# Kernel tuning notes

Measured on AMD Instinct MI355X. Metric: run time of the kernel, lower is better.

## Reference

```python
import jax, jax.numpy as jnp
import numpy as np

B, T, C = 16, 1024, 768
H = 12
D = C // H  # 64 head dim


def setup_inputs() -> dict:
    key = jax.random.key(0)
    k1, k2, k3, k4, k5 = jax.random.split(key, 5)
    s = 0.02
    return {
        "x": jax.random.normal(k1, (B, T, C), dtype=jnp.float32),
        "w_attn": jax.random.normal(k2, (C, 3 * C), dtype=jnp.float32) * s,
        "b_attn": jax.random.normal(k3, (3 * C,), dtype=jnp.float32) * s,
        "w_proj": jax.random.normal(k4, (C, C), dtype=jnp.float32) * s,
        "b_proj": jax.random.normal(k5, (C,), dtype=jnp.float32) * s,
    }


def reference(x, w_attn, b_attn, w_proj, b_proj):
    Bc, Tc, Cc = x.shape
    qkv = x @ w_attn + b_attn  # [B,T,3C]
    q, k, v = jnp.split(qkv, 3, axis=-1)
    # [B,T,C] -> [B,H,T,D]
    q = q.reshape(Bc, Tc, H, D).transpose(0, 2, 1, 3)
    k = k.reshape(Bc, Tc, H, D).transpose(0, 2, 1, 3)
    v = v.reshape(Bc, Tc, H, D).transpose(0, 2, 1, 3)
    scale = 1.0 / np.sqrt(D).astype(np.float32)
    atn = jnp.einsum("bhqd,bhkd->bhqk", q, k) * scale
    causal = jnp.tril(jnp.ones((Tc, Tc), dtype=bool))
    atn = jnp.where(causal[None, None], atn, -jnp.inf)
    atn = jax.nn.softmax(atn, axis=-1)
    y = jnp.einsum("bhqk,bhkd->bhqd", atn, v)
    y = y.transpose(0, 2, 1, 3).reshape(Bc, Tc, Cc)
    return y @ w_proj + b_proj
```

## Files before the change

### kernel.cpp

```cpp
#include <hip/hip_runtime.h>
#include <hip/hip_bf16.h>

typedef __attribute__((ext_vector_type(4))) float f32x4;
typedef __attribute__((ext_vector_type(8))) short s16x8;
typedef __attribute__((ext_vector_type(4))) short s16x4;

#define AS1 __attribute__((address_space(1)))
#define AS3 __attribute__((address_space(3)))

__device__ __forceinline__ short f2bf(float f) {
    union { float f; unsigned u; } a; a.f = f;
    unsigned r = a.u + 0x7fff + ((a.u >> 16) & 1);
    return (short)(r >> 16);
}

__device__ __forceinline__ unsigned pk_bf16(float a, float b) {
    unsigned r;
    asm("v_cvt_pk_bf16_f32 %0, %1, %2" : "=v"(r) : "v"(a), "v"(b));
    return r;
}


__global__ __launch_bounds__(256) void convert_f32_bf16(const float* __restrict__ in,
                                                        short* __restrict__ out, int n4) {
    int i = blockIdx.x * 256 + threadIdx.x;
    if (i < n4) {
        f32x4 v = *(const f32x4*)(in + (long)i * 4);
        s16x4 o;
        o.x = f2bf(v.x); o.y = f2bf(v.y); o.z = f2bf(v.z); o.w = f2bf(v.w);
        *(s16x4*)(out + (long)i * 4) = o;
    }
}

__global__ __launch_bounds__(256) void transpose_w(const float* __restrict__ src,
                                                   short* __restrict__ dst, int K, int N) {
    __shared__ short t[64][65];
    int k0 = blockIdx.x * 64, n0 = blockIdx.y * 64;
    int tid = threadIdx.x;
    for (int i = tid; i < 64 * 64; i += 256) {
        int r = i >> 6, c = i & 63;
        t[r][c] = f2bf(src[(long)(k0 + r) * N + n0 + c]);
    }
    __syncthreads();
    for (int i = tid; i < 64 * 64; i += 256) {
        int r = i >> 6, c = i & 63;
        dst[(long)(n0 + r) * K + k0 + c] = t[c][r];
    }
}


template <int MODE>
__global__ __launch_bounds__(256) void gemm_bt(const short* __restrict__ A,
                                               const short* __restrict__ BT,
                                               const float* __restrict__ bias,
                                               float* __restrict__ outF,
                                               short* __restrict__ q_,
                                               short* __restrict__ k_,
                                               short* __restrict__ v_,
                                               int M, int N, int K) {
    __shared__ short lA[2 * 64 * 64];
    __shared__ short lB[2 * 64 * 64];
    int tid = threadIdx.x;
    int lane = tid & 63, w = tid >> 6;
    int wr = w >> 1, wc = w & 1;
    int lo = lane & 15, hi = lane >> 4;

    int bid = blockIdx.x;
    int swz = (bid & 7) * ((int)gridDim.x >> 3) + (bid >> 3);
    int NX = N >> 7;
    int bx = swz % NX, by = swz / NX;
    int m0 = by * 128, n0 = bx * 128;

    f32x4 acc[4][4];
#pragma unroll
    for (int i = 0; i < 4; ++i)
#pragma unroll
        for (int j = 0; j < 4; ++j) acc[i][j] = (f32x4){0.f, 0.f, 0.f, 0.f};

    const short* Abase = A + (long)m0 * K;
    const short* Bbase = BT + (long)n0 * K;

    int lr = lane >> 3;
    int cc = (lane & 7) ^ lr;
    int growoff = cc >> 2;
    int gcol = (cc & 3) * 8;

    int srlo = lo >> 1;
    int rpar = (lo & 1) << 2;

    for (int k0 = 0; k0 < K; k0 += 64) {
        __syncthreads();
#pragma unroll
        for (int kk = 0; kk < 2; ++kk)
#pragma unroll
            for (int j = 0; j < 2; ++j) {
                int sr = w * 16 + j * 8 + lr;
                long grow = (long)(sr * 2 + growoff);
                const short* ga = Abase + grow * K + k0 + kk * 32 + gcol;
                const short* gb = Bbase + grow * K + k0 + kk * 32 + gcol;
                short* da = lA + kk * 4096 + (w * 16 + j * 8) * 64;
                short* db = lB + kk * 4096 + (w * 16 + j * 8) * 64;
                __builtin_amdgcn_global_load_lds((const AS1 void*)ga, (AS3 void*)da, 16, 0, 0);
                __builtin_amdgcn_global_load_lds((const AS1 void*)gb, (AS3 void*)db, 16, 0, 0);
            }
        __syncthreads();

#pragma unroll
        for (int kk = 0; kk < 2; ++kk) {
            s16x8 a[4], b[4];
#pragma unroll
            for (int mi = 0; mi < 4; ++mi)
                a[mi] = *(const s16x8*)(lA + kk * 4096 + (wr * 32 + mi * 8 + srlo) * 64 +
                                        ((rpar + hi) ^ srlo) * 8);
#pragma unroll
            for (int ni = 0; ni < 4; ++ni)
                b[ni] = *(const s16x8*)(lB + kk * 4096 + (wc * 32 + ni * 8 + srlo) * 64 +
                                        ((rpar + hi) ^ srlo) * 8);
#pragma unroll
            for (int mi = 0; mi < 4; ++mi)
#pragma unroll
                for (int ni = 0; ni < 4; ++ni)
                    acc[mi][ni] = __builtin_amdgcn_mfma_f32_16x16x32_bf16(a[mi], b[ni], acc[mi][ni], 0, 0, 0);
        }
    }

    float bs[4];
#pragma unroll
    for (int ni = 0; ni < 4; ++ni) bs[ni] = bias[n0 + wc * 64 + ni * 16 + lo];

    if (MODE == 1) {
        int blk = (n0 + wc * 64) >> 6;
        int part = (blk >= 24) ? 2 : (blk >= 12 ? 1 : 0);
        int hh = blk - part * 12;
        int bidx = m0 >> 10;
        int trow0 = (m0 & 1023) + wr * 64;
        long gb_ = ((long)(bidx * 12 + hh)) << 16;
        if (part == 2) {
#pragma unroll
            for (int mi = 0; mi < 4; ++mi)
#pragma unroll
                for (int ni = 0; ni < 4; ++ni) {
                    s16x4 o;
                    o.x = f2bf(acc[mi][ni][0] + bs[ni]);
                    o.y = f2bf(acc[mi][ni][1] + bs[ni]);
                    o.z = f2bf(acc[mi][ni][2] + bs[ni]);
                    o.w = f2bf(acc[mi][ni][3] + bs[ni]);
                    int tq = trow0 + mi * 16 + hi * 4;
                    *(s16x4*)(v_ + gb_ + (long)(ni * 16 + lo) * 1024 + tq) = o;
                }
        } else {
            short* dst = (part == 0) ? q_ : k_;
            float scl = (part == 0) ? 0.180336880f : 1.0f;
#pragma unroll
            for (int mi = 0; mi < 4; ++mi)
#pragma unroll
                for (int ni = 0; ni < 4; ++ni)
#pragma unroll
                    for (int r = 0; r < 4; ++r) {
                        int trow = trow0 + mi * 16 + hi * 4 + r;
                        float v = (acc[mi][ni][r] + bs[ni]) * scl;
                        dst[gb_ + (long)trow * 64 + ni * 16 + lo] = f2bf(v);
                    }
        }
    } else {
#pragma unroll
        for (int mi = 0; mi < 4; ++mi)
#pragma unroll
            for (int ni = 0; ni < 4; ++ni)
#pragma unroll
                for (int r = 0; r < 4; ++r) {
                    int gm = m0 + wr * 64 + mi * 16 + hi * 4 + r;
                    int gn = n0 + wc * 64 + ni * 16 + lo;
                    outF[(long)gm * N + gn] = acc[mi][ni][r] + bs[ni];
                }
    }
}


__device__ __forceinline__ void qk_softmax(const short* __restrict__ Kb_,
                                           int kv0, int qb0, bool diag,
                                           s16x8 bq0, s16x8 bq1,
                                           f32x4 (&ov)[4], float& mrun, float& lrun,
                                           s16x8 (&ap)[2],
                                           int lo, int hi, int hi2, int sA, int sB,
                                           int sl0, int sl1) {
    f32x4 s[4];
    __builtin_amdgcn_s_setprio(1);
#pragma unroll
    for (int n = 0; n < 4; ++n) {
        const short* kr = Kb_ + (n * 16 + lo) * 64;
        s16x8 kf0 = *(const s16x8*)(kr + sl0);
        s16x8 kf1 = *(const s16x8*)(kr + sl1);
        f32x4 t = (f32x4){0.f, 0.f, 0.f, 0.f};
        t = __builtin_amdgcn_mfma_f32_16x16x32_bf16(kf0, bq0, t, 0, 0, 0);
        t = __builtin_amdgcn_mfma_f32_16x16x32_bf16(kf1, bq1, t, 0, 0, 0);
        s[n] = t;
    }
    __builtin_amdgcn_s_setprio(0);

    int qglob = qb0 + lo;
    if (diag) {
#pragma unroll
        for (int n = 0; n < 4; ++n)
#pragma unroll
            for (int r = 0; r < 4; ++r)
                if (kv0 + n * 16 + hi * 4 + r > qglob) s[n][r] = -3.0e38f;
    }
    float mx = fmaxf(fmaxf(fmaxf(s[0][0], s[0][1]), fmaxf(s[0][2], s[0][3])),
                     fmaxf(fmaxf(s[1][0], s[1][1]), fmaxf(s[1][2], s[1][3])));
    mx = fmaxf(mx, fmaxf(fmaxf(fmaxf(s[2][0], s[2][1]), fmaxf(s[2][2], s[2][3])),
                         fmaxf(fmaxf(s[3][0], s[3][1]), fmaxf(s[3][2], s[3][3]))));
    mx = fmaxf(mx, __shfl_xor(mx, 16));
    mx = fmaxf(mx, __shfl_xor(mx, 32));
    if (!__all(mx - mrun <= 8.0f)) {
        float mn = fmaxf(mrun, mx);
        float alpha = exp2f(mrun - mn);
        mrun = mn;
        lrun *= alpha;
#pragma unroll
        for (int nd = 0; nd < 4; ++nd)
#pragma unroll
            for (int r = 0; r < 4; ++r) ov[nd][r] *= alpha;
    }
    float m = mrun;
    float rs = 0.f;
#pragma unroll
    for (int n = 0; n < 4; ++n)
#pragma unroll
        for (int r = 0; r < 4; ++r) {
            float p = exp2f(s[n][r] - m);
            s[n][r] = p;
            rs += p;
        }
    rs += __shfl_xor(rs, 16);
    rs += __shfl_xor(rs, 32);
    lrun += rs;

    unsigned W[4][2];
#pragma unroll
    for (int n = 0; n < 4; ++n) {
        W[n][0] = pk_bf16(s[n][0], s[n][1]);
        W[n][1] = pk_bf16(s[n][2], s[n][3]);
    }
#pragma unroll
    for (int kc = 0; kc < 2; ++kc) {
        unsigned a0 = __shfl(W[kc * 2][0], sA), b0 = __shfl(W[kc * 2 + 1][0], sA);
        unsigned a1 = __shfl(W[kc * 2][1], sA), b1 = __shfl(W[kc * 2 + 1][1], sA);
        unsigned a2 = __shfl(W[kc * 2][0], sB), b2 = __shfl(W[kc * 2 + 1][0], sB);
        unsigned a3 = __shfl(W[kc * 2][1], sB), b3 = __shfl(W[kc * 2 + 1][1], sB);
        union { unsigned u[4]; s16x8 v; } cv;
        cv.u[0] = hi2 ? b0 : a0;
        cv.u[1] = hi2 ? b1 : a1;
        cv.u[2] = hi2 ? b2 : a2;
        cv.u[3] = hi2 ? b3 : a3;
        ap[kc] = cv.v;
    }
}

__device__ __forceinline__ void pv_accum(const short* __restrict__ Vb_,
                                         const s16x8 (&ap)[2], f32x4 (&ov)[4],
                                         int lo, int sl0, int sl1) {
    __builtin_amdgcn_s_setprio(1);
#pragma unroll
    for (int nd = 0; nd < 4; ++nd) {
        const short* vr = Vb_ + (nd * 16 + lo) * 64;
        s16x8 av0 = *(const s16x8*)(vr + sl0);
        s16x8 av1 = *(const s16x8*)(vr + sl1);
        ov[nd] = __builtin_amdgcn_mfma_f32_16x16x32_bf16(av0, ap[0], ov[nd], 0, 0, 0);
        ov[nd] = __builtin_amdgcn_mfma_f32_16x16x32_bf16(av1, ap[1], ov[nd], 0, 0, 0);
    }
    __builtin_amdgcn_s_setprio(0);
}

__device__ __forceinline__ void store_out(const f32x4 (&ov)[4], float lrun,
                                          long rowbase, int qb0, int h,
                                          int lo, int hi, short* __restrict__ y) {
    float inv = 1.0f / lrun;
    long row = (rowbase + qb0 + lo) * 768 + h * 64;
#pragma unroll
    for (int nd = 0; nd < 4; ++nd)
#pragma unroll
        for (int j2 = 0; j2 < 2; ++j2) {
            unsigned pv = pk_bf16(ov[nd][2 * j2] * inv, ov[nd][2 * j2 + 1] * inv);
            *(unsigned*)(y + row + nd * 16 + hi * 4 + 2 * j2) = pv;
        }
}

__global__ __launch_bounds__(256) void flash_attn9(const short* __restrict__ qpk,
                                                   const short* __restrict__ kpk,
                                                   const short* __restrict__ vtg,
                                                   short* __restrict__ y) {
    __shared__ short Kb[2][4096];
    __shared__ short Vb[4096];

    int d = blockIdx.x;
    int qp = d / 192, g = d % 192;
    int h = g % 12, b = g / 12;
    int tid = threadIdx.x, lane = tid & 63, w = tid >> 6;
    int lo = lane & 15, hi = lane >> 4, hi2 = hi >> 1;
    long rowbase = (long)b * 1024;
    const short* kb_g = kpk + (long)g * 65536;
    const short* vt_g = vtg + (long)g * 65536;
    int sA = ((hi & 1) * 2) * 16 + lo, sB = sA + 16;

    int rl = lane >> 3;
    int cs8 = (((lane & 7) ^ rl)) * 8;
    int r0 = w * 8 + rl;
    int sl0 = (hi ^ (lo & 7)) * 8;
    int sl1 = ((hi + 4) ^ (lo & 7)) * 8;

    int qbA = qp * 64 + w * 16;
    int qbB = (15 - qp) * 64 + w * 16;

    f32x4 ov[4];
    float mrun = -3.0e38f, lrun = 0.f;
#pragma unroll
    for (int nd = 0; nd < 4; ++nd) ov[nd] = (f32x4){0.f, 0.f, 0.f, 0.f};
    s16x8 bq0, bq1;
    {
        const short* qrow = qpk + ((long)g * 1024 + qbA + lo) * 64;
        bq0 = *(const s16x8*)(qrow + hi * 8);
        bq1 = *(const s16x8*)(qrow + 32 + hi * 8);
    }

#define STAGE_K(kv0_, buf_)                                                                  \
    do {                                                                                     \
        _Pragma("unroll")                                                                    \
        for (int i_ = 0; i_ < 2; ++i_) {                                                     \
            int r_ = i_ * 32 + r0;                                                           \
            __builtin_amdgcn_global_load_lds(                                                \
                (const AS1 void*)(kb_g + (long)((kv0_) + r_) * 64 + cs8),                    \
                (AS3 void*)(Kb[buf_] + (i_ * 32 + w * 8) * 64), 16, 0, 0);                   \
        }                                                                                    \
    } while (0)

#define STAGE_V(kv0_)                                                                        \
    do {                                                                                     \
        _Pragma("unroll")                                                                    \
        for (int i_ = 0; i_ < 2; ++i_) {                                                     \
            int r_ = i_ * 32 + r0;                                                           \
            __builtin_amdgcn_global_load_lds(                                                \
                (const AS1 void*)(vt_g + (long)r_ * 1024 + (kv0_) + cs8),                    \
                (AS3 void*)(Vb + (i_ * 32 + w * 8) * 64), 16, 0, 0);                         \
        }                                                                                    \
    } while (0)

    STAGE_K(0, 0);
    STAGE_V(0);
    __syncthreads();

    int cur = 0;
    for (int u = 0; u < 17; ++u) {
        int nu = u + 1;
        int nkv0 = (nu <= qp) ? nu * 64 : (nu - qp - 1) * 64;
        if (nu < 17) STAGE_K(nkv0, cur ^ 1);

        bool phaseA = (u <= qp);
        int kv0 = phaseA ? u * 64 : (u - qp - 1) * 64;
        int qb0 = phaseA ? qbA : qbB;
        bool diag = phaseA ? (u == qp) : (u == 16);

        s16x8 ap[2];
        qk_softmax(Kb[cur], kv0, qb0, diag, bq0, bq1, ov, mrun, lrun, ap,
                   lo, hi, hi2, sA, sB, sl0, sl1);

        __syncthreads();
        __builtin_amdgcn_sched_barrier(0);

        pv_accum(Vb, ap, ov, lo, sl0, sl1);

        if (phaseA && u == qp) {
            store_out(ov, lrun, rowbase, qbA, h, lo, hi, y);
            const short* qrow = qpk + ((long)g * 1024 + qbB + lo) * 64;
            bq0 = *(const s16x8*)(qrow + hi * 8);
            bq1 = *(const s16x8*)(qrow + 32 + hi * 8);
#pragma unroll
            for (int nd = 0; nd < 4; ++nd) ov[nd] = (f32x4){0.f, 0.f, 0.f, 0.f};
            mrun = -3.0e38f; lrun = 0.f;
        }

        __builtin_amdgcn_s_barrier();
        __builtin_amdgcn_sched_barrier(0);
        if (nu < 17) STAGE_V(nkv0);
        cur ^= 1;
    }
    store_out(ov, lrun, rowbase, qbB, h, lo, hi, y);
#undef STAGE_K
#undef STAGE_V
}


extern "C" void kernel_launch(void* const* d_in, const int* in_sizes, int n_in,
                              void* d_out, int out_size, void* d_ws, size_t ws_size,
                              hipStream_t stream) {
    const float* x      = (const float*)d_in[0];
    const float* w_attn = (const float*)d_in[1];
    const float* b_attn = (const float*)d_in[2];
    const float* w_proj = (const float*)d_in[3];
    const float* b_proj = (const float*)d_in[4];

    char* ws = (char*)d_ws;
    short* x_bf = (short*)ws;
    short* qpk  = (short*)(ws + 25165824);
    short* kpk  = (short*)(ws + 50331648);
    short* vt   = (short*)(ws + 75497472);
    short* yb   = (short*)(ws + 100663296);
    short* waT  = (short*)(ws + 125829120);
    short* wpT  = (short*)(ws + 129368064);

    convert_f32_bf16<<<dim3(12288), dim3(256), 0, stream>>>(x, x_bf, 3145728);
    transpose_w<<<dim3(12, 36), dim3(256), 0, stream>>>(w_attn, waT, 768, 2304);
    transpose_w<<<dim3(12, 12), dim3(256), 0, stream>>>(w_proj, wpT, 768, 768);
    gemm_bt<1><<<dim3(2304), dim3(256), 0, stream>>>(x_bf, waT, b_attn,
                                                     (float*)nullptr, qpk, kpk, vt,
                                                     16384, 2304, 768);
    flash_attn9<<<dim3(1536), dim3(256), 0, stream>>>(qpk, kpk, vt, yb);
    gemm_bt<0><<<dim3(768), dim3(256), 0, stream>>>(yb, wpT, b_proj,
                                                    (float*)d_out, (short*)nullptr,
                                                    (short*)nullptr, (short*)nullptr,
                                                    16384, 768, 768);
}
```

Measured before the change: 201.3 us.

## Double-buffer GEMM LDS tiles to prefetch next K-slice during MFMA

Restructures the GEMM main loop so each 32-wide K slice goes into one of two LDS buffers. The next slice is issued via global_load_lds while the current one is consumed by MFMAs, which removes one barrier per iteration and overlaps memory with compute. It also raises wave priority around the MFMA block with s_setprio. In exchange it runs twice as many loop iterations with smaller K steps, and it relies on a single barrier per iteration to protect buffer reuse.

```diff
diff --git a/kernel.cpp b/kernel.cpp
--- a/kernel.cpp
+++ b/kernel.cpp
@@ -58,8 +58,8 @@
                                                short* __restrict__ k_,
                                                short* __restrict__ v_,
                                                int M, int N, int K) {
-    __shared__ short lA[2 * 64 * 64];
-    __shared__ short lB[2 * 64 * 64];
+    __shared__ short lA[2][64 * 64];
+    __shared__ short lB[2][64 * 64];
     int tid = threadIdx.x;
     int lane = tid & 63, w = tid >> 6;
     int wr = w >> 1, wc = w & 1;
@@ -88,41 +88,50 @@
     int srlo = lo >> 1;
     int rpar = (lo & 1) << 2;
 
-    for (int k0 = 0; k0 < K; k0 += 64) {
+    int T = K >> 5;
+
+#define GSTAGE(tt_, buf_)                                                                   \
+    do {                                                                                    \
+        _Pragma("unroll")                                                                   \
+        for (int j_ = 0; j_ < 2; ++j_) {                                                    \
+            int sr_ = w * 16 + j_ * 8 + lr;                                                 \
+            long grow_ = (long)(sr_ * 2 + growoff);                                         \
+            __builtin_amdgcn_global_load_lds(                                               \
+                (const AS1 void*)(Abase + grow_ * K + (tt_) * 32 + gcol),                   \
+                (AS3 void*)(lA[buf_] + (w * 16 + j_ * 8) * 64), 16, 0, 0);                  \
+            __builtin_amdgcn_global_load_lds(                                               \
+                (const AS1 void*)(Bbase + grow_ * K + (tt_) * 32 + gcol),                   \
+                (AS3 void*)(lB[buf_] + (w * 16 + j_ * 8) * 64), 16, 0, 0);                  \
+        }                                                                                   \
+    } while (0)
+
+    GSTAGE(0, 0);
+    __syncthreads();
+
+    for (int t = 0; t < T; ++t) {
+        int buf = t & 1;
+        if (t + 1 < T) GSTAGE(t + 1, buf ^ 1);
+
+        s16x8 a[4], b[4];
+#pragma unroll
+        for (int mi = 0; mi < 4; ++mi)
+            a[mi] = *(const s16x8*)(lA[buf] + (wr * 32 + mi * 8 + srlo) * 64 +
+                                    ((rpar + hi) ^ srlo) * 8);
+#pragma unroll
+        for (int ni = 0; ni < 4; ++ni)
+            b[ni] = *(const s16x8*)(lB[buf] + (wc * 32 + ni * 8 + srlo) * 64 +
+                                    ((rpar + hi) ^ srlo) * 8);
+        __builtin_amdgcn_s_setprio(1);
+#pragma unroll
+        for (int mi = 0; mi < 4; ++mi)
+#pragma unroll
+            for (int ni = 0; ni < 4; ++ni)
+                acc[mi][ni] = __builtin_amdgcn_mfma_f32_16x16x32_bf16(a[mi], b[ni], acc[mi][ni], 0, 0, 0);
+        __builtin_amdgcn_s_setprio(0);
+
         __syncthreads();
-#pragma unroll
-        for (int kk = 0; kk < 2; ++kk)
-#pragma unroll
-            for (int j = 0; j < 2; ++j) {
-                int sr = w * 16 + j * 8 + lr;
-                long grow = (long)(sr * 2 + growoff);
-                const short* ga = Abase + grow * K + k0 + kk * 32 + gcol;
-                const short* gb = Bbase + grow * K + k0 + kk * 32 + gcol;
-                short* da = lA + kk * 4096 + (w * 16 + j * 8) * 64;
-                short* db = lB + kk * 4096 + (w * 16 + j * 8) * 64;
-                __builtin_amdgcn_global_load_lds((const AS1 void*)ga, (AS3 void*)da, 16, 0, 0);
-                __builtin_amdgcn_global_load_lds((const AS1 void*)gb, (AS3 void*)db, 16, 0, 0);
-            }
-        __syncthreads();
-
-#pragma unroll
-        for (int kk = 0; kk < 2; ++kk) {
-            s16x8 a[4], b[4];
-#pragma unroll
-            for (int mi = 0; mi < 4; ++mi)
-                a[mi] = *(const s16x8*)(lA + kk * 4096 + (wr * 32 + mi * 8 + srlo) * 64 +
-                                        ((rpar + hi) ^ srlo) * 8);
-#pragma unroll
-            for (int ni = 0; ni < 4; ++ni)
-                b[ni] = *(const s16x8*)(lB + kk * 4096 + (wc * 32 + ni * 8 + srlo) * 64 +
-                                        ((rpar + hi) ^ srlo) * 8);
-#pragma unroll
-            for (int mi = 0; mi < 4; ++mi)
-#pragma unroll
-                for (int ni = 0; ni < 4; ++ni)
-                    acc[mi][ni] = __builtin_amdgcn_mfma_f32_16x16x32_bf16(a[mi], b[ni], acc[mi][ni], 0, 0, 0);
-        }
-    }
+    }
+#undef GSTAGE
 
     float bs[4];
 #pragma unroll
```

Result: no change. 204.0 us (+1.3%).

## Replace GEMM with 256x256-tile, 8-wave, double-buffered pipelined kernel

Applied to the files above, without the earlier changes.

Both projection GEMMs now use a new kernel with 256x256 output tiles, 512 threads and 128KB of dynamic LDS split into two buffers. Global-to-LDS loads for the next K-steps are issued between four MFMA phases, with manual waitcnt, barriers and setprio, so memory traffic overlaps with math. The larger tiles are meant to raise data reuse per block and hide load latency. The cost is fewer blocks: 576 for the QKV GEMM and 192 for the output projection. At this LDS size roughly one block fits per CU, which risks wave-quantization tails and leaving CUs idle for the smaller GEMM.

```diff
diff --git a/kernel.cpp b/kernel.cpp
--- a/kernel.cpp
+++ b/kernel.cpp
@@ -50,127 +50,220 @@
 
 
 template <int MODE>
-__global__ __launch_bounds__(256) void gemm_bt(const short* __restrict__ A,
-                                               const short* __restrict__ BT,
-                                               const float* __restrict__ bias,
-                                               float* __restrict__ outF,
-                                               short* __restrict__ q_,
-                                               short* __restrict__ k_,
-                                               short* __restrict__ v_,
-                                               int M, int N, int K) {
-    __shared__ short lA[2 * 64 * 64];
-    __shared__ short lB[2 * 64 * 64];
+__global__ __launch_bounds__(512, 2) void gemm8(const short* __restrict__ A,
+                                                const short* __restrict__ BT,
+                                                const float* __restrict__ bias,
+                                                float* __restrict__ outF,
+                                                short* __restrict__ q_,
+                                                short* __restrict__ k_,
+                                                short* __restrict__ v_,
+                                                int M, int N, int K) {
+    extern __shared__ short smem[];
+    short* lA = smem;
+    short* lB = smem + 32768;
+
     int tid = threadIdx.x;
-    int lane = tid & 63, w = tid >> 6;
-    int wr = w >> 1, wc = w & 1;
+    int lane = tid & 63, wid = tid >> 6;
+    int wm = wid >> 1, wn = wid & 1;
     int lo = lane & 15, hi = lane >> 4;
+    int srlo = lo >> 1, rpar = (lo & 1) << 2;
 
     int bid = blockIdx.x;
     int swz = (bid & 7) * ((int)gridDim.x >> 3) + (bid >> 3);
-    int NX = N >> 7;
+    int NX = N >> 8;
     int bx = swz % NX, by = swz / NX;
-    int m0 = by * 128, n0 = bx * 128;
-
-    f32x4 acc[4][4];
+    int m0 = by * 256, n0 = bx * 256;
+
+    const short* Ag = A + (long)m0 * K;
+    const short* Bg = BT + (long)n0 * K;
+
+    f32x4 acc[4][8];
 #pragma unroll
     for (int i = 0; i < 4; ++i)
 #pragma unroll
-        for (int j = 0; j < 4; ++j) acc[i][j] = (f32x4){0.f, 0.f, 0.f, 0.f};
-
-    const short* Abase = A + (long)m0 * K;
-    const short* Bbase = BT + (long)n0 * K;
-
-    int lr = lane >> 3;
-    int cc = (lane & 7) ^ lr;
-    int growoff = cc >> 2;
-    int gcol = (cc & 3) * 8;
-
-    int srlo = lo >> 1;
-    int rpar = (lo & 1) << 2;
-
-    for (int k0 = 0; k0 < K; k0 += 64) {
-        __syncthreads();
-#pragma unroll
-        for (int kk = 0; kk < 2; ++kk)
-#pragma unroll
-            for (int j = 0; j < 2; ++j) {
-                int sr = w * 16 + j * 8 + lr;
-                long grow = (long)(sr * 2 + growoff);
-                const short* ga = Abase + grow * K + k0 + kk * 32 + gcol;
-                const short* gb = Bbase + grow * K + k0 + kk * 32 + gcol;
-                short* da = lA + kk * 4096 + (w * 16 + j * 8) * 64;
-                short* db = lB + kk * 4096 + (w * 16 + j * 8) * 64;
-                __builtin_amdgcn_global_load_lds((const AS1 void*)ga, (AS3 void*)da, 16, 0, 0);
-                __builtin_amdgcn_global_load_lds((const AS1 void*)gb, (AS3 void*)db, 16, 0, 0);
+        for (int j = 0; j < 8; ++j) acc[i][j] = (f32x4){0.f, 0.f, 0.f, 0.f};
+
+    int srl_ = tid >> 3;
+    int s_ = tid & 7;
+    int cc_ = s_ ^ (srl_ & 7);
+    int gp_ = cc_ >> 2;
+    int gk_ = (cc_ & 3) * 8;
+
+#define STG(Xg_, Xl_, t_, h_)                                                               \
+    do {                                                                                    \
+        int srg_ = (h_) * 64 + srl_;                                                        \
+        long grow_ = (long)(srg_ * 2 + gp_);                                                \
+        const short* s0_ = (Xg_) + grow_ * K + (t_) * 64 + gk_;                             \
+        __builtin_amdgcn_global_load_lds((const AS1 void*)s0_,                              \
+                                         (AS3 void*)((Xl_) + srg_ * 64 + s_ * 8), 16, 0, 0);\
+        __builtin_amdgcn_global_load_lds((const AS1 void*)(s0_ + 32),                       \
+                                         (AS3 void*)((Xl_) + 8192 + srg_ * 64 + s_ * 8),    \
+                                         16, 0, 0);                                         \
+    } while (0)
+
+    int T = K >> 6;
+
+    STG(Ag, lA, 0, 0); STG(Ag, lA, 0, 1);
+    STG(Bg, lB, 0, 0); STG(Bg, lB, 0, 1);
+    if (T > 1) {
+        STG(Ag, lA + 16384, 1, 0); STG(Ag, lA + 16384, 1, 1);
+        STG(Bg, lB + 16384, 1, 0);
+    }
+    asm volatile("s_waitcnt vmcnt(6)" ::: "memory");
+    __builtin_amdgcn_s_barrier();
+
+    int soff = ((rpar + hi) ^ srlo) * 8;
+
+    for (int j = 0; j < T; ++j) {
+        int b = j & 1;
+        short* lAb = lA + b * 16384;
+        short* lBb = lB + b * 16384;
+        short* lAn = lA + (b ^ 1) * 16384;
+        short* lBn = lB + (b ^ 1) * 16384;
+
+        s16x8 a[4][2], b01[2][2];
+#pragma unroll
+        for (int mi = 0; mi < 4; ++mi)
+#pragma unroll
+            for (int kk = 0; kk < 2; ++kk)
+                a[mi][kk] = *(const s16x8*)(lAb + (kk * 128 + wm * 32 + mi * 8 + srlo) * 64 + soff);
+#pragma unroll
+        for (int ni = 0; ni < 2; ++ni)
+#pragma unroll
+            for (int kk = 0; kk < 2; ++kk)
+                b01[ni][kk] = *(const s16x8*)(lBb + (kk * 128 + wn * 64 + ni * 8 + srlo) * 64 + soff);
+        if (j + 1 < T) STG(Bg, lBn, j + 1, 1);
+        __builtin_amdgcn_s_barrier();
+        asm volatile("s_waitcnt lgkmcnt(0)" ::: "memory");
+        __builtin_amdgcn_sched_barrier(0);
+        __builtin_amdgcn_s_setprio(1);
+#pragma unroll
+        for (int mi = 0; mi < 4; ++mi)
+#pragma unroll
+            for (int ni = 0; ni < 2; ++ni)
+#pragma unroll
+                for (int kk = 0; kk < 2; ++kk)
+                    acc[mi][ni] = __builtin_amdgcn_mfma_f32_16x16x32_bf16(a[mi][kk], b01[ni][kk], acc[mi][ni], 0, 0, 0);
+        __builtin_amdgcn_s_setprio(0);
+        __builtin_amdgcn_s_barrier();
+
+        s16x8 b23[2][2];
+#pragma unroll
+        for (int ni = 0; ni < 2; ++ni)
+#pragma unroll
+            for (int kk = 0; kk < 2; ++kk)
+                b23[ni][kk] = *(const s16x8*)(lBb + (kk * 128 + wn * 64 + (ni + 2) * 8 + srlo) * 64 + soff);
+        if (j + 2 < T) STG(Ag, lAb, j + 2, 0);
+        __builtin_amdgcn_s_barrier();
+        asm volatile("s_waitcnt lgkmcnt(0)" ::: "memory");
+        __builtin_amdgcn_sched_barrier(0);
+        __builtin_amdgcn_s_setprio(1);
+#pragma unroll
+        for (int mi = 0; mi < 4; ++mi)
+#pragma unroll
+            for (int ni = 0; ni < 2; ++ni)
+#pragma unroll
+                for (int kk = 0; kk < 2; ++kk)
+                    acc[mi][2 + ni] = __builtin_amdgcn_mfma_f32_16x16x32_bf16(a[mi][kk], b23[ni][kk], acc[mi][2 + ni], 0, 0, 0);
+        __builtin_amdgcn_s_setprio(0);
+        __builtin_amdgcn_s_barrier();
+
+        s16x8 b45[2][2], b67[2][2];
+#pragma unroll
+        for (int ni = 0; ni < 2; ++ni)
+#pragma unroll
+            for (int kk = 0; kk < 2; ++kk) {
+                b45[ni][kk] = *(const s16x8*)(lBb + (kk * 128 + wn * 64 + (ni + 4) * 8 + srlo) * 64 + soff);
+                b67[ni][kk] = *(const s16x8*)(lBb + (kk * 128 + wn * 64 + (ni + 6) * 8 + srlo) * 64 + soff);
             }
-        __syncthreads();
-
-#pragma unroll
-        for (int kk = 0; kk < 2; ++kk) {
-            s16x8 a[4], b[4];
-#pragma unroll
-            for (int mi = 0; mi < 4; ++mi)
-                a[mi] = *(const s16x8*)(lA + kk * 4096 + (wr * 32 + mi * 8 + srlo) * 64 +
-                                        ((rpar + hi) ^ srlo) * 8);
-#pragma unroll
-            for (int ni = 0; ni < 4; ++ni)
-                b[ni] = *(const s16x8*)(lB + kk * 4096 + (wc * 32 + ni * 8 + srlo) * 64 +
-                                        ((rpar + hi) ^ srlo) * 8);
-#pragma unroll
-            for (int mi = 0; mi < 4; ++mi)
-#pragma unroll
-                for (int ni = 0; ni < 4; ++ni)
-                    acc[mi][ni] = __builtin_amdgcn_mfma_f32_16x16x32_bf16(a[mi], b[ni], acc[mi][ni], 0, 0, 0);
+        if (j + 2 < T) STG(Ag, lAb, j + 2, 1);
+        __builtin_amdgcn_s_barrier();
+        asm volatile("s_waitcnt lgkmcnt(0)" ::: "memory");
+        __builtin_amdgcn_sched_barrier(0);
+        __builtin_amdgcn_s_setprio(1);
+#pragma unroll
+        for (int mi = 0; mi < 4; ++mi)
+#pragma unroll
+            for (int ni = 0; ni < 2; ++ni)
+#pragma unroll
+                for (int kk = 0; kk < 2; ++kk)
+                    acc[mi][4 + ni] = __builtin_amdgcn_mfma_f32_16x16x32_bf16(a[mi][kk], b45[ni][kk], acc[mi][4 + ni], 0, 0, 0);
+        __builtin_amdgcn_s_setprio(0);
+        __builtin_amdgcn_s_barrier();
+
+        if (j + 2 < T) {
+            STG(Bg, lBb, j + 2, 0);
+            asm volatile("s_waitcnt vmcnt(6)" ::: "memory");
+        } else if (j + 1 < T) {
+            asm volatile("s_waitcnt vmcnt(0)" ::: "memory");
         }
-    }
-
-    float bs[4];
-#pragma unroll
-    for (int ni = 0; ni < 4; ++ni) bs[ni] = bias[n0 + wc * 64 + ni * 16 + lo];
+        __builtin_amdgcn_s_barrier();
+        __builtin_amdgcn_s_setprio(1);
+#pragma unroll
+        for (int mi = 0; mi < 4; ++mi)
+#pragma unroll
+            for (int ni = 0; ni < 2; ++ni)
+#pragma unroll
+                for (int kk = 0; kk < 2; ++kk)
+                    acc[mi][6 + ni] = __builtin_amdgcn_mfma_f32_16x16x32_bf16(a[mi][kk], b67[ni][kk], acc[mi][6 + ni], 0, 0, 0);
+        __builtin_amdgcn_s_setprio(0);
+        __builtin_amdgcn_s_barrier();
+    }
+#undef STG
+
+    float bs[8];
+#pragma unroll
+    for (int ni = 0; ni < 8; ++ni) bs[ni] = bias[n0 + wn * 128 + ni * 16 + lo];
 
     if (MODE == 1) {
-        int blk = (n0 + wc * 64) >> 6;
-        int part = (blk >= 24) ? 2 : (blk >= 12 ? 1 : 0);
-        int hh = blk - part * 12;
         int bidx = m0 >> 10;
-        int trow0 = (m0 & 1023) + wr * 64;
-        long gb_ = ((long)(bidx * 12 + hh)) << 16;
-        if (part == 2) {
-#pragma unroll
-            for (int mi = 0; mi < 4; ++mi)
-#pragma unroll
-                for (int ni = 0; ni < 4; ++ni) {
-                    s16x4 o;
-                    o.x = f2bf(acc[mi][ni][0] + bs[ni]);
-                    o.y = f2bf(acc[mi][ni][1] + bs[ni]);
-                    o.z = f2bf(acc[mi][ni][2] + bs[ni]);
-                    o.w = f2bf(acc[mi][ni][3] + bs[ni]);
-                    int tq = trow0 + mi * 16 + hi * 4;
-                    *(s16x4*)(v_ + gb_ + (long)(ni * 16 + lo) * 1024 + tq) = o;
-                }
-        } else {
-            short* dst = (part == 0) ? q_ : k_;
-            float scl = (part == 0) ? 0.180336880f : 1.0f;
-#pragma unroll
-            for (int mi = 0; mi < 4; ++mi)
-#pragma unroll
-                for (int ni = 0; ni < 4; ++ni)
-#pragma unroll
-                    for (int r = 0; r < 4; ++r) {
-                        int trow = trow0 + mi * 16 + hi * 4 + r;
-                        float v = (acc[mi][ni][r] + bs[ni]) * scl;
-                        dst[gb_ + (long)trow * 64 + ni * 16 + lo] = f2bf(v);
+        int trow0 = (m0 & 1023) + wm * 64;
+#pragma unroll
+        for (int nh = 0; nh < 2; ++nh) {
+            int blk = ((n0 + wn * 128) >> 6) + nh;
+            int part = (blk >= 24) ? 2 : (blk >= 12 ? 1 : 0);
+            int hh = blk - part * 12;
+            long gb_ = ((long)(bidx * 12 + hh)) << 16;
+            if (part == 2) {
+#pragma unroll
+                for (int mi = 0; mi < 4; ++mi)
+#pragma unroll
+                    for (int n2 = 0; n2 < 4; ++n2) {
+                        int ni = nh * 4 + n2;
+                        s16x4 o;
+                        o.x = f2bf(acc[mi][ni][0] + bs[ni]);
+                        o.y = f2bf(acc[mi][ni][1] + bs[ni]);
+                        o.z = f2bf(acc[mi][ni][2] + bs[ni]);
+                        o.w = f2bf(acc[mi][ni][3] + bs[ni]);
+                        int tq = trow0 + mi * 16 + hi * 4;
+                        *(s16x4*)(v_ + gb_ + (long)(n2 * 16 + lo) * 1024 + tq) = o;
                     }
+            } else {
+                short* dst = (part == 0) ? q_ : k_;
+                float scl = (part == 0) ? 0.180336880f : 1.0f;
+#pragma unroll
+                for (int mi = 0; mi < 4; ++mi)
+#pragma unroll
+                    for (int n2 = 0; n2 < 4; ++n2) {
+                        int ni = nh * 4 + n2;
+#pragma unroll
+                        for (int r = 0; r < 4; ++r) {
+                            int trow = trow0 + mi * 16 + hi * 4 + r;
+                            float v = (acc[mi][ni][r] + bs[ni]) * scl;
+                            dst[gb_ + (long)trow * 64 + n2 * 16 + lo] = f2bf(v);
+                        }
+                    }
+            }
         }
     } else {
 #pragma unroll
         for (int mi = 0; mi < 4; ++mi)
 #pragma unroll
-            for (int ni = 0; ni < 4; ++ni)
+            for (int ni = 0; ni < 8; ++ni)
 #pragma unroll
                 for (int r = 0; r < 4; ++r) {
-                    int gm = m0 + wr * 64 + mi * 16 + hi * 4 + r;
-                    int gn = n0 + wc * 64 + ni * 16 + lo;
+                    int gm = m0 + wm * 64 + mi * 16 + hi * 4 + r;
+                    int gn = n0 + wn * 128 + ni * 16 + lo;
                     outF[(long)gm * N + gn] = acc[mi][ni][r] + bs[ni];
                 }
     }
@@ -408,15 +501,20 @@
     short* waT  = (short*)(ws + 125829120);
     short* wpT  = (short*)(ws + 129368064);
 
+    hipFuncSetAttribute(reinterpret_cast<const void*>(&gemm8<1>),
+                        hipFuncAttributeMaxDynamicSharedMemorySize, 131072);
+    hipFuncSetAttribute(reinterpret_cast<const void*>(&gemm8<0>),
+                        hipFuncAttributeMaxDynamicSharedMemorySize, 131072);
+
     convert_f32_bf16<<<dim3(12288), dim3(256), 0, stream>>>(x, x_bf, 3145728);
     transpose_w<<<dim3(12, 36), dim3(256), 0, stream>>>(w_attn, waT, 768, 2304);
     transpose_w<<<dim3(12, 12), dim3(256), 0, stream>>>(w_proj, wpT, 768, 768);
-    gemm_bt<1><<<dim3(2304), dim3(256), 0, stream>>>(x_bf, waT, b_attn,
-                                                     (float*)nullptr, qpk, kpk, vt,
-                                                     16384, 2304, 768);
+    gemm8<1><<<dim3(576), dim3(512), 131072, stream>>>(x_bf, waT, b_attn,
+                                                       (float*)nullptr, qpk, kpk, vt,
+                                                       16384, 2304, 768);
     flash_attn9<<<dim3(1536), dim3(256), 0, stream>>>(qpk, kpk, vt, yb);
-    gemm_bt<0><<<dim3(768), dim3(256), 0, stream>>>(yb, wpT, b_proj,
-                                                    (float*)d_out, (short*)nullptr,
-                                                    (short*)nullptr, (short*)nullptr,
-                                                    16384, 768, 768);
-}
+    gemm8<0><<<dim3(192), dim3(512), 131072, stream>>>(yb, wpT, b_proj,
+                                                       (float*)d_out, (short*)nullptr,
+                                                       (short*)nullptr, (short*)nullptr,
+                                                       16384, 768, 768);
+}
```

New measurement: 205.3 us. Within noise of the previous version (+2.0%).
